# Optimization experiments

Hardware: AMD Instinct MI355X
Metric: run time of the kernel (lower is better)

## Reference

```python
import jax, jax.numpy as jnp
import numpy as np

IN_DIM = 512
OUT_DIM = 512
NUM_HARMONICS = 32
BATCH = 4096


def setup_inputs() -> dict:
    key = jax.random.key(0)
    k1, k2 = jax.random.split(key)
    x = jax.random.normal(k1, (BATCH, IN_DIM), dtype=jnp.float32)
    std = 1.0 / np.sqrt(IN_DIM * NUM_HARMONICS)
    fourier_coeffs = jax.random.normal(
        k2, (IN_DIM, NUM_HARMONICS, 2, OUT_DIM), dtype=jnp.float32) * std
    bias = jnp.zeros((OUT_DIM,), dtype=jnp.float32)
    return {"x": x, "fourier_coeffs": fourier_coeffs, "bias": bias}


def reference(x, fourier_coeffs, bias):
    # k = [1, ..., num_harmonics]
    k = jnp.arange(1, fourier_coeffs.shape[1] + 1, dtype=x.dtype)
    kx = x[:, :, None] * k                      # [b, i, g]
    trig = jnp.stack([jnp.cos(kx), jnp.sin(kx)], axis=-1)  # [b, i, g, 2]
    out = jnp.einsum('bigf,igfo->bo', trig, fourier_coeffs)
    return out + bias
```

## Files before the change

### kernel.cpp

```cpp
#include <hip/hip_runtime.h>
#include <hip/hip_bf16.h>
#include <stdint.h>
#include <stddef.h>

#define BATCH   4096
#define INDIM   512
#define OUTDIM  512
#define NH      32
#define KKDIM   64
#define INV2PI  0.15915494309189535f

#define BM       128
#define BN       128
#define THREADS  256
#define KSPLIT   8
#define DIMS_PER_WG (INDIM / KSPLIT)
#define CHUNK_COLS  256
#define CHUNK_ELEMS (CHUNK_COLS * KKDIM)

#define B_BYTES       16384
#define OFF_X         (2 * B_BYTES)
#define X_CHUNK_BYTES (8 * BM * 4)
#define SMEM_BYTES    (OFF_X + 2 * X_CHUNK_BYTES)

typedef short  bhalf8  __attribute__((ext_vector_type(8)));
typedef float  vfloat4 __attribute__((ext_vector_type(4)));

union AFrag { uint4 u; bhalf8 h; };

__device__ __forceinline__ unsigned pack_bf16(float a, float b) {
    union { __hip_bfloat162 h2; unsigned u; } cv;
    cv.h2 = __float22bfloat162_rn(float2{a, b});
    return cv.u;
}

__device__ __forceinline__ void async_copy16(const void* gsrc, void* ldst) {
    __builtin_amdgcn_global_load_lds(
        (const __attribute__((address_space(1))) void*)(uintptr_t)gsrc,
        (__attribute__((address_space(3))) void*)(uint32_t)(uintptr_t)ldst,
        16, 0, 0);
}

__global__ __launch_bounds__(256) void fkan_prepass(const float* __restrict__ coeffs,
                                                    unsigned short* __restrict__ Bt) {
    __shared__ float lds[64][260];
    const int t  = threadIdx.x;
    const int cb = blockIdx.x & 1;
    const int i  = blockIdx.x >> 1;
    const float* __restrict__ src = coeffs + (size_t)i * (KKDIM * OUTDIM) + cb * CHUNK_COLS;
    unsigned short* __restrict__ chunk = Bt + (size_t)(cb * INDIM + i) * CHUNK_ELEMS;
#pragma unroll
    for (int rd = 0; rd < 16; ++rd) {
        const int r  = rd * 4 + (t >> 6);
        const int c4 = (t & 63) * 4;
        const float4 v = *(const float4*)(src + (size_t)r * OUTDIM + c4);
        *(float4*)&lds[r][c4] = v;
    }
    __syncthreads();
#pragma unroll
    for (int s = 0; s < 8; ++s) {
        const int unit = t + s * 256;
        const int col  = unit >> 3;
        const int pc   = unit & 7;
        const int kb   = (pc ^ (col & 7)) * 8;
        uint4 o;
        o.x = pack_bf16(lds[kb + 0][col], lds[kb + 1][col]);
        o.y = pack_bf16(lds[kb + 2][col], lds[kb + 3][col]);
        o.z = pack_bf16(lds[kb + 4][col], lds[kb + 5][col]);
        o.w = pack_bf16(lds[kb + 6][col], lds[kb + 7][col]);
        ((uint4*)chunk)[unit] = o;
    }
}

__global__ __launch_bounds__(256) void fkan_bias_init(const float* __restrict__ bias,
                                                      float* __restrict__ out) {
    const int idx = blockIdx.x * 256 + threadIdx.x;
    ((float4*)out)[idx] = ((const float4*)bias)[idx & 127];
}

__device__ __forceinline__ void stage_B(const char* __restrict__ chunk_half, char* smem,
                                        int parity, int t) {
    char* bdst = smem + parity * B_BYTES;
#pragma unroll
    for (int s = 0; s < 4; ++s) {
        const int unit = t + s * 256;
        async_copy16(chunk_half + unit * 16, bdst + unit * 16);
    }
}

__device__ __forceinline__ void stage_x(const float* __restrict__ x, char* smem,
                                        int rowbase, int dimbase, int cn, int t) {
    const int r  = t >> 1;
    const int d0 = (t & 1) * 4;
    const float4 xv = *(const float4*)(x + (size_t)(rowbase + r) * INDIM + dimbase + cn * 8 + d0);
    float* xr = (float*)(smem + OFF_X + (cn & 1) * X_CHUNK_BYTES);
    xr[(d0 + 0) * BM + r] = xv.x * INV2PI;
    xr[(d0 + 1) * BM + r] = xv.y * INV2PI;
    xr[(d0 + 2) * BM + r] = xv.z * INV2PI;
    xr[(d0 + 3) * BM + r] = xv.w * INV2PI;
}

__global__ __launch_bounds__(THREADS, 4) void fkan_main(const float* __restrict__ x,
                                                        const unsigned short* __restrict__ Bt,
                                                        float* __restrict__ out) {
    __shared__ char smem[SMEM_BYTES];
    const int t      = threadIdx.x;
    const int grp    = blockIdx.x & 31;
    const int member = blockIdx.x >> 5;
    const int kq      = grp & 7;
    const int cb4     = grp >> 3;
    const int cb2     = cb4 >> 1;
    const int rowbase = member * BM;
    const int colbase = cb4 * BN;
    const int dimbase = kq * DIMS_PER_WG;

    const int lane = t & 63;
    const int w    = t >> 6;
    const int fr   = lane & 15;
    const int fq   = lane >> 4;
    const int fx   = lane & 7;

    const float k0f = (float)(fq * 4 + 1);
    const float k1f = (float)(fq * 4 + 17);

    const char* __restrict__ chunkbase =
        (const char*)(Bt + (size_t)(cb2 * INDIM + dimbase) * CHUNK_ELEMS) + (cb4 & 1) * 16384;

    vfloat4 acc[2][8];
#pragma unroll
    for (int a = 0; a < 2; ++a)
#pragma unroll
        for (int b = 0; b < 8; ++b) acc[a][b] = (vfloat4)0.0f;

    stage_x(x, smem, rowbase, dimbase, 0, t);
    stage_B(chunkbase, smem, 0, t);
    __syncthreads();

#pragma unroll 2
    for (int it = 0; it < DIMS_PER_WG; ++it) {
        const int p    = it & 1;
        const int inxt = it + 1;
        if (inxt < DIMS_PER_WG)
            stage_B(chunkbase + (size_t)inxt * 32768, smem, inxt & 1, t);
        if ((it & 7) == 0) {
            const int cn = (it >> 3) + 1;
            if (cn < 8) stage_x(x, smem, rowbase, dimbase, cn, t);
        }

        const float* xr = (const float*)(smem + OFF_X + ((it >> 3) & 1) * X_CHUNK_BYTES)
                          + (it & 7) * BM;
        bhalf8 av0[2], av1[2];
#pragma unroll
        for (int rt = 0; rt < 2; ++rt) {
            const float rv = xr[w * 32 + rt * 16 + fr];
            const float cd = __builtin_amdgcn_cosf(rv);
            const float sd = __builtin_amdgcn_sinf(rv);
            AFrag A;
            float c = __builtin_amdgcn_cosf(k0f * rv);
            float s = __builtin_amdgcn_sinf(k0f * rv);
            A.u.x = pack_bf16(c, s);
            { const float nc = c*cd - s*sd, ns = s*cd + c*sd; c = nc; s = ns; }
            A.u.y = pack_bf16(c, s);
            { const float nc = c*cd - s*sd, ns = s*cd + c*sd; c = nc; s = ns; }
            A.u.z = pack_bf16(c, s);
            { const float nc = c*cd - s*sd, ns = s*cd + c*sd; c = nc; s = ns; }
            A.u.w = pack_bf16(c, s);
            av0[rt] = A.h;
            c = __builtin_amdgcn_cosf(k1f * rv);
            s = __builtin_amdgcn_sinf(k1f * rv);
            A.u.x = pack_bf16(c, s);
            { const float nc = c*cd - s*sd, ns = s*cd + c*sd; c = nc; s = ns; }
            A.u.y = pack_bf16(c, s);
            { const float nc = c*cd - s*sd, ns = s*cd + c*sd; c = nc; s = ns; }
            A.u.z = pack_bf16(c, s);
            { const float nc = c*cd - s*sd, ns = s*cd + c*sd; c = nc; s = ns; }
            A.u.w = pack_bf16(c, s);
            av1[rt] = A.h;
        }

        const char* Bb = smem + p * B_BYTES;
        __builtin_amdgcn_s_setprio(1);
#pragma unroll
        for (int ct = 0; ct < 8; ++ct) {
            const int cbyte = (ct * 16 + fr) * 128;
            const bhalf8 b0 = *(const bhalf8*)(Bb + cbyte + ((fq ^ fx) * 16));
            acc[0][ct] = __builtin_amdgcn_mfma_f32_16x16x32_bf16(av0[0], b0, acc[0][ct], 0, 0, 0);
            acc[1][ct] = __builtin_amdgcn_mfma_f32_16x16x32_bf16(av0[1], b0, acc[1][ct], 0, 0, 0);
            const bhalf8 b1 = *(const bhalf8*)(Bb + cbyte + (((4 + fq) ^ fx) * 16));
            acc[0][ct] = __builtin_amdgcn_mfma_f32_16x16x32_bf16(av1[0], b1, acc[0][ct], 0, 0, 0);
            acc[1][ct] = __builtin_amdgcn_mfma_f32_16x16x32_bf16(av1[1], b1, acc[1][ct], 0, 0, 0);
        }
        __builtin_amdgcn_s_setprio(0);
        __syncthreads();
    }

#pragma unroll
    for (int rt = 0; rt < 2; ++rt) {
#pragma unroll
        for (int ct = 0; ct < 8; ++ct) {
            const int col  = colbase + ct * 16 + fr;
            const int row0 = rowbase + w * 32 + rt * 16 + fq * 4;
#pragma unroll
            for (int r = 0; r < 4; ++r)
                atomicAdd(out + (size_t)(row0 + r) * OUTDIM + col, acc[rt][ct][r]);
        }
    }
}

__global__ __launch_bounds__(256) void fkan_naive(const float* __restrict__ x,
                                                  const float* __restrict__ coeffs,
                                                  const float* __restrict__ bias,
                                                  float* __restrict__ out) {
    const int b = blockIdx.x >> 1;
    const int o = ((blockIdx.x & 1) << 8) + threadIdx.x;
    float acc = bias[o];
    const float* xrow = x + (size_t)b * INDIM;
    for (int i = 0; i < INDIM; ++i) {
        const float rv = xrow[i] * INV2PI;
        const float cd = __builtin_amdgcn_cosf(rv);
        const float sd = __builtin_amdgcn_sinf(rv);
        float c = cd, s = sd;
        const float* cp = coeffs + (size_t)i * (KKDIM * OUTDIM) + o;
#pragma unroll 4
        for (int g = 0; g < NH; ++g) {
            acc += c * cp[g * 2 * OUTDIM] + s * cp[(g * 2 + 1) * OUTDIM];
            const float nc = c * cd - s * sd;
            const float ns = s * cd + c * sd;
            c = nc; s = ns;
        }
    }
    out[(size_t)b * OUTDIM + o] = acc;
}

extern "C" void kernel_launch(void* const* d_in, const int* in_sizes, int n_in,
                              void* d_out, int out_size, void* d_ws, size_t ws_size,
                              hipStream_t stream) {
    (void)in_sizes; (void)n_in; (void)out_size;
    const float* x      = (const float*)d_in[0];
    const float* coeffs = (const float*)d_in[1];
    const float* bias   = (const float*)d_in[2];
    float* out          = (float*)d_out;

    const size_t bt_bytes = (size_t)2 * INDIM * CHUNK_ELEMS * sizeof(unsigned short);
    if (ws_size >= bt_bytes) {
        unsigned short* Bt = (unsigned short*)d_ws;
        fkan_prepass<<<2 * INDIM, 256, 0, stream>>>(coeffs, Bt);
        fkan_bias_init<<<(BATCH * OUTDIM) / (4 * 256), 256, 0, stream>>>(bias, out);
        fkan_main<<<(BATCH / BM) * (OUTDIM / BN) * KSPLIT, THREADS, 0, stream>>>(x, Bt, out);
    } else {
        fkan_naive<<<BATCH * 2, 256, 0, stream>>>(x, coeffs, bias, out);
    }
}
```

Measured before the change: 279.3 us.

## Software-pipeline trig A-fragment generation and load x directly from global

Removes the LDS staging of x and has each lane read its own x value straight from global memory. The loop is manually unrolled by two with explicit double-buffered A fragments, so the sin/cos fragments for the next dimension are computed while the MFMAs for the current one run. Launch bounds drop from 4 to 3 waves-per-SIMD hint, giving more registers for the extra fragment set at the cost of occupancy. The global x loads are uncoalesced scalar reads (stride INDIM) and may add latency.

New measurement: 287.2 us. 2.8% more time.

```diff
diff --git a/kernel.cpp b/kernel.cpp
--- a/kernel.cpp
+++ b/kernel.cpp
@@ -19,9 +19,7 @@
 #define CHUNK_ELEMS (CHUNK_COLS * KKDIM)
 
 #define B_BYTES       16384
-#define OFF_X         (2 * B_BYTES)
-#define X_CHUNK_BYTES (8 * BM * 4)
-#define SMEM_BYTES    (OFF_X + 2 * X_CHUNK_BYTES)
+#define SMEM_BYTES    (2 * B_BYTES)
 
 typedef short  bhalf8  __attribute__((ext_vector_type(8)));
 typedef float  vfloat4 __attribute__((ext_vector_type(4)));
@@ -88,19 +86,52 @@
     }
 }
 
-__device__ __forceinline__ void stage_x(const float* __restrict__ x, char* smem,
-                                        int rowbase, int dimbase, int cn, int t) {
-    const int r  = t >> 1;
-    const int d0 = (t & 1) * 4;
-    const float4 xv = *(const float4*)(x + (size_t)(rowbase + r) * INDIM + dimbase + cn * 8 + d0);
-    float* xr = (float*)(smem + OFF_X + (cn & 1) * X_CHUNK_BYTES);
-    xr[(d0 + 0) * BM + r] = xv.x * INV2PI;
-    xr[(d0 + 1) * BM + r] = xv.y * INV2PI;
-    xr[(d0 + 2) * BM + r] = xv.z * INV2PI;
-    xr[(d0 + 3) * BM + r] = xv.w * INV2PI;
-}
-
-__global__ __launch_bounds__(THREADS, 4) void fkan_main(const float* __restrict__ x,
+__device__ __forceinline__ void make_av(float rv, float k0f, float k1f,
+                                        bhalf8* a0, bhalf8* a1) {
+    const float cd = __builtin_amdgcn_cosf(rv);
+    const float sd = __builtin_amdgcn_sinf(rv);
+    AFrag A;
+    float c = __builtin_amdgcn_cosf(k0f * rv);
+    float s = __builtin_amdgcn_sinf(k0f * rv);
+    A.u.x = pack_bf16(c, s);
+    { const float nc = c*cd - s*sd, ns = s*cd + c*sd; c = nc; s = ns; }
+    A.u.y = pack_bf16(c, s);
+    { const float nc = c*cd - s*sd, ns = s*cd + c*sd; c = nc; s = ns; }
+    A.u.z = pack_bf16(c, s);
+    { const float nc = c*cd - s*sd, ns = s*cd + c*sd; c = nc; s = ns; }
+    A.u.w = pack_bf16(c, s);
+    *a0 = A.h;
+    c = __builtin_amdgcn_cosf(k1f * rv);
+    s = __builtin_amdgcn_sinf(k1f * rv);
+    A.u.x = pack_bf16(c, s);
+    { const float nc = c*cd - s*sd, ns = s*cd + c*sd; c = nc; s = ns; }
+    A.u.y = pack_bf16(c, s);
+    { const float nc = c*cd - s*sd, ns = s*cd + c*sd; c = nc; s = ns; }
+    A.u.z = pack_bf16(c, s);
+    { const float nc = c*cd - s*sd, ns = s*cd + c*sd; c = nc; s = ns; }
+    A.u.w = pack_bf16(c, s);
+    *a1 = A.h;
+}
+
+#define MFMA_BLOCK(Bb, A0, A1)                                                  \
+    do {                                                                        \
+        _Pragma("unroll")                                                       \
+        for (int ct = 0; ct < 8; ++ct) {                                        \
+            const int cbyte = (ct * 16 + fr) * 128;                             \
+            const bhalf8 b0 = *(const bhalf8*)((Bb) + cbyte + off0);            \
+            acc[0][ct] = __builtin_amdgcn_mfma_f32_16x16x32_bf16(               \
+                (A0)[0], b0, acc[0][ct], 0, 0, 0);                              \
+            acc[1][ct] = __builtin_amdgcn_mfma_f32_16x16x32_bf16(               \
+                (A0)[1], b0, acc[1][ct], 0, 0, 0);                              \
+            const bhalf8 b1 = *(const bhalf8*)((Bb) + cbyte + off1);            \
+            acc[0][ct] = __builtin_amdgcn_mfma_f32_16x16x32_bf16(               \
+                (A1)[0], b1, acc[0][ct], 0, 0, 0);                              \
+            acc[1][ct] = __builtin_amdgcn_mfma_f32_16x16x32_bf16(               \
+                (A1)[1], b1, acc[1][ct], 0, 0, 0);                              \
+        }                                                                       \
+    } while (0)
+
+__global__ __launch_bounds__(THREADS, 3) void fkan_main(const float* __restrict__ x,
                                                         const unsigned short* __restrict__ Bt,
                                                         float* __restrict__ out) {
     __shared__ char smem[SMEM_BYTES];
@@ -119,10 +150,15 @@
     const int fr   = lane & 15;
     const int fq   = lane >> 4;
     const int fx   = lane & 7;
+    const int off0 = (fq ^ fx) * 16;
+    const int off1 = ((4 + fq) ^ fx) * 16;
 
     const float k0f = (float)(fq * 4 + 1);
     const float k1f = (float)(fq * 4 + 17);
 
+    const float* __restrict__ xp0 = x + (size_t)(rowbase + w * 32 + fr) * INDIM + dimbase;
+    const float* __restrict__ xp1 = xp0 + (size_t)16 * INDIM;
+
     const char* __restrict__ chunkbase =
         (const char*)(Bt + (size_t)(cb2 * INDIM + dimbase) * CHUNK_ELEMS) + (cb4 & 1) * 16384;
 
@@ -132,66 +168,31 @@
 #pragma unroll
         for (int b = 0; b < 8; ++b) acc[a][b] = (vfloat4)0.0f;
 
-    stage_x(x, smem, rowbase, dimbase, 0, t);
+    bhalf8 a0A[2], a1A[2], a0B[2], a1B[2];
     stage_B(chunkbase, smem, 0, t);
+    make_av(xp0[0] * INV2PI, k0f, k1f, &a0A[0], &a1A[0]);
+    make_av(xp1[0] * INV2PI, k0f, k1f, &a0A[1], &a1A[1]);
     __syncthreads();
 
-#pragma unroll 2
-    for (int it = 0; it < DIMS_PER_WG; ++it) {
-        const int p    = it & 1;
-        const int inxt = it + 1;
-        if (inxt < DIMS_PER_WG)
-            stage_B(chunkbase + (size_t)inxt * 32768, smem, inxt & 1, t);
-        if ((it & 7) == 0) {
-            const int cn = (it >> 3) + 1;
-            if (cn < 8) stage_x(x, smem, rowbase, dimbase, cn, t);
-        }
-
-        const float* xr = (const float*)(smem + OFF_X + ((it >> 3) & 1) * X_CHUNK_BYTES)
-                          + (it & 7) * BM;
-        bhalf8 av0[2], av1[2];
-#pragma unroll
-        for (int rt = 0; rt < 2; ++rt) {
-            const float rv = xr[w * 32 + rt * 16 + fr];
-            const float cd = __builtin_amdgcn_cosf(rv);
-            const float sd = __builtin_amdgcn_sinf(rv);
-            AFrag A;
-            float c = __builtin_amdgcn_cosf(k0f * rv);
-            float s = __builtin_amdgcn_sinf(k0f * rv);
-            A.u.x = pack_bf16(c, s);
-            { const float nc = c*cd - s*sd, ns = s*cd + c*sd; c = nc; s = ns; }
-            A.u.y = pack_bf16(c, s);
-            { const float nc = c*cd - s*sd, ns = s*cd + c*sd; c = nc; s = ns; }
-            A.u.z = pack_bf16(c, s);
-            { const float nc = c*cd - s*sd, ns = s*cd + c*sd; c = nc; s = ns; }
-            A.u.w = pack_bf16(c, s);
-            av0[rt] = A.h;
-            c = __builtin_amdgcn_cosf(k1f * rv);
-            s = __builtin_amdgcn_sinf(k1f * rv);
-            A.u.x = pack_bf16(c, s);
-            { const float nc = c*cd - s*sd, ns = s*cd + c*sd; c = nc; s = ns; }
-            A.u.y = pack_bf16(c, s);
-            { const float nc = c*cd - s*sd, ns = s*cd + c*sd; c = nc; s = ns; }
-            A.u.z = pack_bf16(c, s);
-            { const float nc = c*cd - s*sd, ns = s*cd + c*sd; c = nc; s = ns; }
-            A.u.w = pack_bf16(c, s);
-            av1[rt] = A.h;
-        }
-
-        const char* Bb = smem + p * B_BYTES;
-        __builtin_amdgcn_s_setprio(1);
-#pragma unroll
-        for (int ct = 0; ct < 8; ++ct) {
-            const int cbyte = (ct * 16 + fr) * 128;
-            const bhalf8 b0 = *(const bhalf8*)(Bb + cbyte + ((fq ^ fx) * 16));
-            acc[0][ct] = __builtin_amdgcn_mfma_f32_16x16x32_bf16(av0[0], b0, acc[0][ct], 0, 0, 0);
-            acc[1][ct] = __builtin_amdgcn_mfma_f32_16x16x32_bf16(av0[1], b0, acc[1][ct], 0, 0, 0);
-            const bhalf8 b1 = *(const bhalf8*)(Bb + cbyte + (((4 + fq) ^ fx) * 16));
-            acc[0][ct] = __builtin_amdgcn_mfma_f32_16x16x32_bf16(av1[0], b1, acc[0][ct], 0, 0, 0);
-            acc[1][ct] = __builtin_amdgcn_mfma_f32_16x16x32_bf16(av1[1], b1, acc[1][ct], 0, 0, 0);
-        }
-        __builtin_amdgcn_s_setprio(0);
-        __syncthreads();
+    for (int it2 = 0; it2 < DIMS_PER_WG; it2 += 2) {
+        {
+            const int inxt = it2 + 1;
+            stage_B(chunkbase + (size_t)inxt * 32768, smem, 1, t);
+            make_av(xp0[inxt] * INV2PI, k0f, k1f, &a0B[0], &a1B[0]);
+            make_av(xp1[inxt] * INV2PI, k0f, k1f, &a0B[1], &a1B[1]);
+            MFMA_BLOCK(smem, a0A, a1A);
+            __syncthreads();
+        }
+        {
+            const int inxt = it2 + 2;
+            if (inxt < DIMS_PER_WG) {
+                stage_B(chunkbase + (size_t)inxt * 32768, smem, 0, t);
+                make_av(xp0[inxt] * INV2PI, k0f, k1f, &a0A[0], &a1A[0]);
+                make_av(xp1[inxt] * INV2PI, k0f, k1f, &a0A[1], &a1A[1]);
+            }
+            MFMA_BLOCK(smem + B_BYTES, a0B, a1B);
+            __syncthreads();
+        }
     }
 
 #pragma unroll
```
